# Optimization experiments

Measured on AMD Instinct MI355X. Metric: run time of the kernel, lower is better.

The kernel has to match this reference:

```python
import jax, jax.numpy as jnp
import numpy as np

NEG_SLOPE = 0.01  # nn.LeakyReLU default


def setup_inputs() -> dict:
    key = jax.random.key(0)
    k1, k2, k3, k4, k5, k6 = jax.random.split(key, 6)
    N, E, F_IN, F_OUT = 50000, 800000, 256, 64
    x = jax.random.normal(k1, (N, F_IN), dtype=jnp.float32)
    src = jax.random.randint(k2, (E,), 0, N, dtype=jnp.int32)
    dst = jax.random.randint(k3, (E,), 0, N, dtype=jnp.int32)
    # nn.init.normal_(weight, 0, 0.5) for both Linear layers (no bias)
    W1 = 0.5 * jax.random.normal(k4, (F_OUT, F_IN), dtype=jnp.float32)
    W2 = 0.5 * jax.random.normal(k5, (F_OUT, F_OUT), dtype=jnp.float32)
    # detGAT.a = torch.rand(2*out_feats, 1)
    a = jax.random.uniform(k6, (2 * F_OUT, 1), dtype=jnp.float32)
    return {"x": x, "W1": W1, "W2": W2, "a": a, "src": src, "dst": dst}


def reference(x, W1, W2, a, src, dst):
    N, d = x.shape[0], W1.shape[0]
    # model_base: linear -> (dropout, identity in eval) -> relu, twice
    z = jax.nn.relu(x @ W1.T)
    h = jax.nn.relu(z @ W2.T)  # [N, d]
    # detGAT edge score: LeakyReLU(concat([h_dst, h_src]) @ a)
    # split a so we compute per-node dot products once instead of an [E, 2d] concat
    a_dst, a_src = a[:d, 0], a[d:, 0]
    s_dst = h @ a_dst  # [N]
    s_src = h @ a_src  # [N]
    score = jax.nn.leaky_relu(s_dst[dst] + s_src[src], NEG_SLOPE)  # [E]
    # edge_softmax: softmax over incoming edges of each destination node
    m = jax.ops.segment_max(score, dst, num_segments=N)  # [N]
    e = jnp.exp(score - m[dst])
    ssum = jax.ops.segment_sum(e, dst, num_segments=N)  # [N]
    w = e / ssum[dst]  # [E]
    # weighted scatter-sum of src features to dst nodes
    res = jax.ops.segment_sum(h[src] * w[:, None], dst, num_segments=N)  # [N, d]
    return jax.nn.relu(h - res)
```

## Files before the change

### kernel.cpp

```cpp
#include <hip/hip_runtime.h>
#include <math.h>

#define F_IN 256
#define F_OUT 64
#define NEG_SLOPE 0.01f
#define CAP 8192
#define NB2 256

typedef unsigned short ushort8_t __attribute__((ext_vector_type(8)));
typedef __bf16 bf16x8 __attribute__((ext_vector_type(8)));
typedef float f32x16 __attribute__((ext_vector_type(16)));

__device__ inline unsigned short f2bf(float f) {
    unsigned u = __float_as_uint(f);
    u += 0x7FFF + ((u >> 16) & 1);
    return (unsigned short)(u >> 16);
}
__device__ inline float bf2f(unsigned short u) {
    return __uint_as_float(((unsigned)u) << 16);
}
__device__ inline void splitbf(float x, unsigned short& hi, unsigned short& lo) {
    hi = f2bf(x);
    lo = f2bf(x - bf2f(hi));
}
__device__ inline bf16x8 asbf8(ushort8_t u) {
    union { ushort8_t u; bf16x8 b; } c; c.u = u; return c.b;
}
__device__ inline void split8(const float4& p0, const float4& p1, bf16x8& ah, bf16x8& al) {
    ushort8_t h, l;
    unsigned short th, tl;
    splitbf(p0.x, th, tl); h[0] = th; l[0] = tl;
    splitbf(p0.y, th, tl); h[1] = th; l[1] = tl;
    splitbf(p0.z, th, tl); h[2] = th; l[2] = tl;
    splitbf(p0.w, th, tl); h[3] = th; l[3] = tl;
    splitbf(p1.x, th, tl); h[4] = th; l[4] = tl;
    splitbf(p1.y, th, tl); h[5] = th; l[5] = tl;
    splitbf(p1.z, th, tl); h[6] = th; l[6] = tl;
    splitbf(p1.w, th, tl); h[7] = th; l[7] = tl;
    ah = asbf8(h); al = asbf8(l);
}
__device__ inline float redq32(float v) {
    v += __shfl_xor(v, 1);  v += __shfl_xor(v, 2);  v += __shfl_xor(v, 4);
    v += __shfl_xor(v, 8);  v += __shfl_xor(v, 16);
    return v;
}

__global__ __launch_bounds__(1024)
void prep_scatter_kernel(const float* __restrict__ W1, const float* __restrict__ W2,
                         unsigned short* __restrict__ w1fh, unsigned short* __restrict__ w1fl,
                         unsigned short* __restrict__ w2fh, unsigned short* __restrict__ w2fl,
                         const int* __restrict__ src, const int* __restrict__ dst,
                         int* __restrict__ cursor, int* __restrict__ edata,
                         int E, int chunk)
{
    __shared__ int lh[256], lbase[256], lcur[256];
    const int tid = threadIdx.x;

    if (blockIdx.x < 16) {
        int idx = blockIdx.x * 1024 + tid;
        int jj = idx & 7, l = (idx >> 3) & 63, t = idx >> 9;
        {
            int nt = t & 1, gks = t >> 1;
            int f = nt * 32 + (l & 31);
            int k = gks * 16 + (l >> 5) * 8 + jj;
            unsigned short hi, lo;
            splitbf(W1[f * F_IN + k], hi, lo);
            w1fh[idx] = hi; w1fl[idx] = lo;
        }
        if (idx < 4096) {
            int nt = t & 1, ks = t >> 1;
            int f = nt * 32 + (l & 31);
            int j = ks * 16 + (l >> 5) * 8 + jj;
            unsigned short hi, lo;
            splitbf(W2[f * F_OUT + j], hi, lo);
            w2fh[idx] = hi; w2fl[idx] = lo;
        }
        return;
    }

    const int bid = blockIdx.x - 16;
    if (tid < 256) lh[tid] = 0;
    __syncthreads();
    const int beg = bid * chunk;
    const int end = min(E, beg + chunk);
    for (int i = beg + tid; i < end; i += 1024)
        atomicAdd(&lh[((unsigned)dst[i]) >> 8], 1);
    __syncthreads();
    if (tid < 256) {
        int c = lh[tid];
        lbase[tid] = c ? atomicAdd(&cursor[tid], c) : 0;
        lcur[tid] = 0;
    }
    __syncthreads();
    for (int i = beg + tid; i < end; i += 1024) {
        int d = dst[i];
        int s = src[i];
        int b = ((unsigned)d) >> 8;
        int rk = atomicAdd(&lcur[b], 1);
        edata[b * CAP + lbase[b] + rk] = ((d & 0xFF) << 16) | s;
    }
}

__global__ __launch_bounds__(256)
void mlp_sort_kernel(const float* __restrict__ x,
                     const unsigned short* __restrict__ w1fh,
                     const unsigned short* __restrict__ w1fl,
                     const unsigned short* __restrict__ w2fh,
                     const unsigned short* __restrict__ w2fl,
                     const float* __restrict__ a,
                     unsigned short* __restrict__ hb,
                     float* __restrict__ sdst,
                     float* __restrict__ ssrc, int N,
                     const int* __restrict__ cursor,
                     const int* __restrict__ edata,
                     int* __restrict__ ssorted,
                     int* __restrict__ cnt, int* __restrict__ offs,
                     int MLPB)
{
    __shared__ __align__(16) unsigned short zbuf[4 * 4224];
    __shared__ int hist[256];
    __shared__ int excl[256];

    const int tid = threadIdx.x;
    const int lane = tid & 63;

    if (blockIdx.x < MLPB) {
        const int wid = __builtin_amdgcn_readfirstlane(tid >> 6);
        const int ml = lane & 31;
        const int q = lane >> 5;
        const int node0w = blockIdx.x * 128 + wid * 32;

        unsigned short* zh = zbuf + wid * 4224;
        unsigned short* zl = zh + 2112;

        const int rowc = min(node0w + ml, N - 1);
        const float* __restrict__ xrow = x + (size_t)rowc * F_IN + q * 8;

        f32x16 acc0, acc1;
#pragma unroll
        for (int i = 0; i < 16; i++) { acc0[i] = 0.f; acc1[i] = 0.f; }

        float4 p0 = *(const float4*)(xrow);
        float4 p1 = *(const float4*)(xrow + 4);
        ushort8_t b0h = *(const ushort8_t*)(w1fh + (lane) * 8);
        ushort8_t b0l = *(const ushort8_t*)(w1fl + (lane) * 8);
        ushort8_t b1h = *(const ushort8_t*)(w1fh + (64 + lane) * 8);
        ushort8_t b1l = *(const ushort8_t*)(w1fl + (64 + lane) * 8);

#pragma unroll
        for (int gks = 0; gks < 16; gks++) {
            const int nx = gks < 15 ? gks + 1 : 15;
            float4 q0 = *(const float4*)(xrow + nx * 16);
            float4 q1 = *(const float4*)(xrow + nx * 16 + 4);
            ushort8_t c0h = *(const ushort8_t*)(w1fh + ((nx * 2 + 0) * 64 + lane) * 8);
            ushort8_t c0l = *(const ushort8_t*)(w1fl + ((nx * 2 + 0) * 64 + lane) * 8);
            ushort8_t c1h = *(const ushort8_t*)(w1fh + ((nx * 2 + 1) * 64 + lane) * 8);
            ushort8_t c1l = *(const ushort8_t*)(w1fl + ((nx * 2 + 1) * 64 + lane) * 8);

            bf16x8 ah, al;
            split8(p0, p1, ah, al);
            acc0 = __builtin_amdgcn_mfma_f32_32x32x16_bf16(ah, asbf8(b0h), acc0, 0, 0, 0);
            acc0 = __builtin_amdgcn_mfma_f32_32x32x16_bf16(ah, asbf8(b0l), acc0, 0, 0, 0);
            acc0 = __builtin_amdgcn_mfma_f32_32x32x16_bf16(al, asbf8(b0h), acc0, 0, 0, 0);
            acc1 = __builtin_amdgcn_mfma_f32_32x32x16_bf16(ah, asbf8(b1h), acc1, 0, 0, 0);
            acc1 = __builtin_amdgcn_mfma_f32_32x32x16_bf16(ah, asbf8(b1l), acc1, 0, 0, 0);
            acc1 = __builtin_amdgcn_mfma_f32_32x32x16_bf16(al, asbf8(b1h), acc1, 0, 0, 0);

            p0 = q0; p1 = q1;
            b0h = c0h; b0l = c0l; b1h = c1h; b1l = c1l;
        }

#pragma unroll
        for (int reg = 0; reg < 16; reg++) {
            int nd = (reg & 3) + 8 * (reg >> 2) + 4 * q;
            float z0 = fmaxf(acc0[reg], 0.f);
            float z1 = fmaxf(acc1[reg], 0.f);
            unsigned short h_, l_;
            splitbf(z0, h_, l_);
            zh[nd * 66 + ml] = h_; zl[nd * 66 + ml] = l_;
            splitbf(z1, h_, l_);
            zh[nd * 66 + 32 + ml] = h_; zl[nd * 66 + 32 + ml] = l_;
        }

        f32x16 hacc0, hacc1;
#pragma unroll
        for (int i = 0; i < 16; i++) { hacc0[i] = 0.f; hacc1[i] = 0.f; }
#pragma unroll
        for (int ks = 0; ks < 4; ks++) {
            ushort8_t wh0 = *(const ushort8_t*)(w2fh + ((ks * 2 + 0) * 64 + lane) * 8);
            ushort8_t wl0 = *(const ushort8_t*)(w2fl + ((ks * 2 + 0) * 64 + lane) * 8);
            ushort8_t wh1 = *(const ushort8_t*)(w2fh + ((ks * 2 + 1) * 64 + lane) * 8);
            ushort8_t wl1 = *(const ushort8_t*)(w2fl + ((ks * 2 + 1) * 64 + lane) * 8);
            bf16x8 ah = asbf8(*(const ushort8_t*)(zh + ml * 66 + ks * 16 + q * 8));
            bf16x8 al = asbf8(*(const ushort8_t*)(zl + ml * 66 + ks * 16 + q * 8));
            hacc0 = __builtin_amdgcn_mfma_f32_32x32x16_bf16(ah, asbf8(wh0), hacc0, 0, 0, 0);
            hacc0 = __builtin_amdgcn_mfma_f32_32x32x16_bf16(ah, asbf8(wl0), hacc0, 0, 0, 0);
            hacc0 = __builtin_amdgcn_mfma_f32_32x32x16_bf16(al, asbf8(wh0), hacc0, 0, 0, 0);
            hacc1 = __builtin_amdgcn_mfma_f32_32x32x16_bf16(ah, asbf8(wh1), hacc1, 0, 0, 0);
            hacc1 = __builtin_amdgcn_mfma_f32_32x32x16_bf16(ah, asbf8(wl1), hacc1, 0, 0, 0);
            hacc1 = __builtin_amdgcn_mfma_f32_32x32x16_bf16(al, asbf8(wh1), hacc1, 0, 0, 0);
        }

        const float aD0 = a[ml],            aD1 = a[32 + ml];
        const float aS0 = a[F_OUT + ml],    aS1 = a[F_OUT + 32 + ml];

        float sdv = 0.f, ssv = 0.f;
#pragma unroll
        for (int reg = 0; reg < 16; reg++) {
            int nd = (reg & 3) + 8 * (reg >> 2) + 4 * q;
            float h0 = fmaxf(hacc0[reg], 0.f);
            float h1 = fmaxf(hacc1[reg], 0.f);
            float td = redq32(h0 * aD0 + h1 * aD1);
            float ts = redq32(h0 * aS0 + h1 * aS1);
            if (ml == nd) { sdv = td; ssv = ts; }
            int gn = node0w + nd;
            if (gn < N) {
                hb[(size_t)gn * F_OUT + ml]      = f2bf(h0);
                hb[(size_t)gn * F_OUT + 32 + ml] = f2bf(h1);
            }
        }
        {
            int gn = node0w + ml;
            if ((((ml >> 2) & 1) == q) && gn < N) {
                sdst[gn] = sdv;
                ssrc[gn] = ssv;
            }
        }
        return;
    }

    const int cb = blockIdx.x - MLPB;
    const int base = cb * CAP;
    const int ecnt = cursor[cb];

    hist[tid] = 0;
    __syncthreads();
    for (int i = tid; i < ecnt; i += 256)
        atomicAdd(&hist[((unsigned)edata[base + i]) >> 16], 1);
    __syncthreads();

    if (tid < 64) {
        int v0 = hist[lane * 4], v1 = hist[lane * 4 + 1];
        int v2 = hist[lane * 4 + 2], v3 = hist[lane * 4 + 3];
        int ts = v0 + v1 + v2 + v3;
        int s = ts;
#pragma unroll
        for (int d = 1; d < 64; d <<= 1) {
            int t = __shfl_up(s, d);
            if (lane >= d) s += t;
        }
        int e = s - ts;
        excl[lane * 4] = e;
        excl[lane * 4 + 1] = e + v0;
        excl[lane * 4 + 2] = e + v0 + v1;
        excl[lane * 4 + 3] = e + v0 + v1 + v2;
    }
    __syncthreads();

    {
        int d = cb * 256 + tid;
        if (d < N) {
            cnt[d] = hist[tid];
            offs[d] = base + excl[tid];
        }
    }
    __syncthreads();

    for (int i = tid; i < ecnt; i += 256) {
        int pack = edata[base + i];
        int low = ((unsigned)pack) >> 16;
        int rk = atomicAdd(&excl[low], 1);
        ssorted[base + rk] = pack & 0xFFFF;
    }
}

__global__ __launch_bounds__(256)
void aggregate_kernel(const unsigned short* __restrict__ hb,
                      const float* __restrict__ sdst,
                      const float* __restrict__ ssrc,
                      const int* __restrict__ offs,
                      const int* __restrict__ cnt,
                      const int* __restrict__ ssorted,
                      float* __restrict__ out, int N)
{
    __shared__ float2 ws_sh[4][64];
    const int lane = threadIdx.x & 63;
    const int wid = threadIdx.x >> 6;
    const int d = blockIdx.x * 4 + wid;
    if (d >= N) return;

    const int off = offs[d];
    const int deg = cnt[d];
    const float sdd = sdst[d];
    float M = -INFINITY, S = 0.f, res = 0.f;

    for (int cb = 0; cb < deg; cb += 64) {
        int ce = min(64, deg - cb);
        float score = -INFINITY;
        int s = 0;
        if (lane < ce) {
            s = ssorted[off + cb + lane];
            float sc = sdd + ssrc[s];
            score = sc > 0.f ? sc : NEG_SLOPE * sc;
        }
        float mc = score;
#pragma unroll
        for (int dd = 32; dd > 0; dd >>= 1)
            mc = fmaxf(mc, __shfl_xor(mc, dd));
        float newM = fmaxf(M, mc);
        float scale = __expf(M - newM);
        float w = (lane < ce) ? __expf(score - newM) : 0.f;
        ws_sh[wid][lane] = make_float2(w, __int_as_float(s));
        float csum = w;
#pragma unroll
        for (int dd = 32; dd > 0; dd >>= 1)
            csum += __shfl_xor(csum, dd);
        S = S * scale + csum;
        __builtin_amdgcn_wave_barrier();

        float c[8];
#pragma unroll
        for (int i = 0; i < 8; i++) c[i] = 0.f;
        const int ceo = (ce + 7) & ~7;
        for (int e = 0; e < ceo; e += 8) {
#pragma unroll
            for (int i = 0; i < 8; i++) {
                float2 t = ws_sh[wid][e + i];
                int se = __builtin_amdgcn_readfirstlane(__float_as_int(t.y));
                c[i] = fmaf(t.x, bf2f(hb[((unsigned)se << 6) + lane]), c[i]);
            }
        }
        float t = ((c[0] + c[1]) + (c[2] + c[3])) + ((c[4] + c[5]) + (c[6] + c[7]));
        res = res * scale + t;
        __builtin_amdgcn_wave_barrier();
        M = newM;
    }

    float hf = bf2f(hb[((unsigned)d << 6) + lane]);
    float r = (S > 0.f) ? (hf - res / S) : hf;
    out[(size_t)d * F_OUT + lane] = r > 0.f ? r : 0.f;
}

extern "C" void kernel_launch(void* const* d_in, const int* in_sizes, int n_in,
                              void* d_out, int out_size, void* d_ws,
                              size_t ws_size, hipStream_t stream)
{
    const float* x  = (const float*)d_in[0];
    const float* W1 = (const float*)d_in[1];
    const float* W2 = (const float*)d_in[2];
    const float* a  = (const float*)d_in[3];
    const int* src  = (const int*)d_in[4];
    const int* dst  = (const int*)d_in[5];
    const int N = in_sizes[0] / F_IN;
    const int E = in_sizes[4];

    float* ws = (float*)d_ws;
    float* sdst = ws;
    float* ssrc = sdst + N;
    unsigned short* w1fh = (unsigned short*)(ssrc + N);
    unsigned short* w1fl = w1fh + 16384;
    unsigned short* w2fh = w1fl + 16384;
    unsigned short* w2fl = w2fh + 4096;
    unsigned short* hb = w2fl + 4096;
    int* cnt    = (int*)(hb + (size_t)N * F_OUT);
    int* offs   = cnt + N;
    int* cursor = offs + N;
    int* edata  = cursor + 256;
    int* ssorted = edata + 196 * CAP;

    const int nbc = (N + 255) >> 8;
    const int MLPB = (N + 127) >> 7;
    const int chunk = (E + NB2 - 1) / NB2;

    hipMemsetAsync(cursor, 0, 256 * sizeof(int), stream);
    prep_scatter_kernel<<<16 + NB2, 1024, 0, stream>>>(W1, W2, w1fh, w1fl, w2fh, w2fl,
                                                       src, dst, cursor, edata, E, chunk);
    mlp_sort_kernel<<<MLPB + nbc, 256, 0, stream>>>(x, w1fh, w1fl, w2fh, w2fl, a,
                                                    hb, sdst, ssrc, N,
                                                    cursor, edata, ssorted, cnt, offs,
                                                    MLPB);
    aggregate_kernel<<<(N + 3) / 4, 256, 0, stream>>>(hb, sdst, ssrc, offs, cnt,
                                                      ssorted, (float*)d_out, N);
}
```

Before: 152.9 us.

## Process four destination nodes per wavefront with vectorized feature gathers

The aggregation kernel now gives each destination node a 16-lane group instead of a full 64-lane wave, so one wave handles four nodes. Each lane covers four features and fetches them with a ushort4 load. The softmax reductions shrink to 16-lane shuffles, and the output is written as float4. The aim is to stop wasting most lanes in 64-edge chunks when the average degree is about 16, and to cut per-edge load instructions. In exchange, groups in one wave can diverge when node degrees differ, and padded edges always run 16 gather iterations.

```diff
diff --git a/kernel.cpp b/kernel.cpp
--- a/kernel.cpp
+++ b/kernel.cpp
@@ -284,61 +284,80 @@
                       float* __restrict__ out, int N)
 {
     __shared__ float2 ws_sh[4][64];
-    const int lane = threadIdx.x & 63;
-    const int wid = threadIdx.x >> 6;
-    const int d = blockIdx.x * 4 + wid;
-    if (d >= N) return;
-
-    const int off = offs[d];
-    const int deg = cnt[d];
-    const float sdd = sdst[d];
-    float M = -INFINITY, S = 0.f, res = 0.f;
-
-    for (int cb = 0; cb < deg; cb += 64) {
-        int ce = min(64, deg - cb);
+    const int tid = threadIdx.x;
+    const int lane = tid & 63;
+    const int wid = tid >> 6;
+    const int g = lane >> 4;
+    const int li = lane & 15;
+    const int d = blockIdx.x * 16 + wid * 4 + g;
+    const bool vd = d < N;
+
+    const int off = vd ? offs[d] : 0;
+    const int deg = vd ? cnt[d] : 0;
+    const float sdd = vd ? sdst[d] : 0.f;
+
+    float M = -INFINITY, S = 0.f;
+    float c0 = 0.f, c1 = 0.f, c2 = 0.f, c3 = 0.f;
+
+    for (int cb = 0; cb < deg; cb += 16) {
+        int ce = min(16, deg - cb);
         float score = -INFINITY;
         int s = 0;
-        if (lane < ce) {
-            s = ssorted[off + cb + lane];
+        if (li < ce) {
+            s = ssorted[off + cb + li];
             float sc = sdd + ssrc[s];
             score = sc > 0.f ? sc : NEG_SLOPE * sc;
         }
         float mc = score;
-#pragma unroll
-        for (int dd = 32; dd > 0; dd >>= 1)
-            mc = fmaxf(mc, __shfl_xor(mc, dd));
+        mc = fmaxf(mc, __shfl_xor(mc, 1));
+        mc = fmaxf(mc, __shfl_xor(mc, 2));
+        mc = fmaxf(mc, __shfl_xor(mc, 4));
+        mc = fmaxf(mc, __shfl_xor(mc, 8));
         float newM = fmaxf(M, mc);
         float scale = __expf(M - newM);
-        float w = (lane < ce) ? __expf(score - newM) : 0.f;
+        float w = (li < ce) ? __expf(score - newM) : 0.f;
         ws_sh[wid][lane] = make_float2(w, __int_as_float(s));
         float csum = w;
-#pragma unroll
-        for (int dd = 32; dd > 0; dd >>= 1)
-            csum += __shfl_xor(csum, dd);
+        csum += __shfl_xor(csum, 1);
+        csum += __shfl_xor(csum, 2);
+        csum += __shfl_xor(csum, 4);
+        csum += __shfl_xor(csum, 8);
         S = S * scale + csum;
         __builtin_amdgcn_wave_barrier();
 
-        float c[8];
-#pragma unroll
-        for (int i = 0; i < 8; i++) c[i] = 0.f;
-        const int ceo = (ce + 7) & ~7;
-        for (int e = 0; e < ceo; e += 8) {
-#pragma unroll
-            for (int i = 0; i < 8; i++) {
-                float2 t = ws_sh[wid][e + i];
-                int se = __builtin_amdgcn_readfirstlane(__float_as_int(t.y));
-                c[i] = fmaf(t.x, bf2f(hb[((unsigned)se << 6) + lane]), c[i]);
-            }
-        }
-        float t = ((c[0] + c[1]) + (c[2] + c[3])) + ((c[4] + c[5]) + (c[6] + c[7]));
-        res = res * scale + t;
+        float t0 = 0.f, t1 = 0.f, t2 = 0.f, t3 = 0.f;
+#pragma unroll
+        for (int e = 0; e < 16; e++) {
+            float2 tw = ws_sh[wid][g * 16 + e];
+            int se = __float_as_int(tw.y);
+            ushort4 r = *(const ushort4*)(hb + (((size_t)(unsigned)se) << 6) + li * 4);
+            t0 = fmaf(tw.x, bf2f(r.x), t0);
+            t1 = fmaf(tw.x, bf2f(r.y), t1);
+            t2 = fmaf(tw.x, bf2f(r.z), t2);
+            t3 = fmaf(tw.x, bf2f(r.w), t3);
+        }
+        c0 = c0 * scale + t0;
+        c1 = c1 * scale + t1;
+        c2 = c2 * scale + t2;
+        c3 = c3 * scale + t3;
         __builtin_amdgcn_wave_barrier();
         M = newM;
     }
 
-    float hf = bf2f(hb[((unsigned)d << 6) + lane]);
-    float r = (S > 0.f) ? (hf - res / S) : hf;
-    out[(size_t)d * F_OUT + lane] = r > 0.f ? r : 0.f;
+    if (vd) {
+        ushort4 hr = *(const ushort4*)(hb + (((size_t)(unsigned)d) << 6) + li * 4);
+        float inv = (S > 0.f) ? 1.f / S : 0.f;
+        float r0 = bf2f(hr.x) - c0 * inv;
+        float r1 = bf2f(hr.y) - c1 * inv;
+        float r2 = bf2f(hr.z) - c2 * inv;
+        float r3 = bf2f(hr.w) - c3 * inv;
+        float4 o;
+        o.x = r0 > 0.f ? r0 : 0.f;
+        o.y = r1 > 0.f ? r1 : 0.f;
+        o.z = r2 > 0.f ? r2 : 0.f;
+        o.w = r3 > 0.f ? r3 : 0.f;
+        *(float4*)(out + (size_t)d * F_OUT + li * 4) = o;
+    }
 }
 
 extern "C" void kernel_launch(void* const* d_in, const int* in_sizes, int n_in,
@@ -379,6 +398,6 @@
                                                     hb, sdst, ssrc, N,
                                                     cursor, edata, ssorted, cnt, offs,
                                                     MLPB);
-    aggregate_kernel<<<(N + 3) / 4, 256, 0, stream>>>(hb, sdst, ssrc, offs, cnt,
-                                                      ssorted, (float*)d_out, N);
-}
+    aggregate_kernel<<<(N + 15) / 16, 256, 0, stream>>>(hb, sdst, ssrc, offs, cnt,
+                                                        ssorted, (float*)d_out, N);
+}
```

Measured after the change: 146.1 us. -4.4%, faster.
